# Performance work log

Measured on AMD Instinct MI355X. Metric: run time of the kernel, lower is better.

The kernel has to match this reference:

```python
import jax, jax.numpy as jnp
import numpy as np

N, F, H, E_DIM, G, NE = 20000, 128, 256, 128, 64, 320000

def _ln(x, g, b, eps=1e-5):
    m = jnp.mean(x, axis=-1, keepdims=True)
    v = jnp.mean((x - m) ** 2, axis=-1, keepdims=True)
    return (x - m) * jax.lax.rsqrt(v + eps) * g + b

def _gcn(x, src, dst, W, b, n):
    # GCNConv: h = D^{-1/2}(A+I)D^{-1/2} (x W) + b, degrees from A+I
    h = x @ W
    loop = jnp.arange(n)
    s = jnp.concatenate([src, loop])
    d = jnp.concatenate([dst, loop])
    deg = jax.ops.segment_sum(jnp.ones_like(s, dtype=h.dtype), d, num_segments=n)
    dinv = jax.lax.rsqrt(jnp.maximum(deg, 1.0))
    w_e = dinv[s] * dinv[d]  # [E+N]
    out = jax.ops.segment_sum(h[s] * w_e[:, None], d, num_segments=n)
    return out + b

def setup_inputs() -> dict:
    key = jax.random.key(0)
    ks = jax.random.split(key, 32)
    def nrm(k, shp, scale=0.05):
        return jax.random.normal(k, shp, dtype=jnp.float32) * scale
    inp = {
        'x': jax.random.normal(ks[0], (N, F), dtype=jnp.float32),
        'edge_index': jax.random.randint(ks[1], (2, NE), 0, N),
        'batch': jnp.sort(jax.random.randint(ks[2], (N,), 0, G)),
        'enc_w': nrm(ks[3], (F, H)), 'enc_b': jnp.zeros((H,), jnp.float32),
        'enc_g': jnp.ones((H,), jnp.float32), 'enc_be': jnp.zeros((H,), jnp.float32),
        'w1': nrm(ks[4], (H, H)), 'b1': jnp.zeros((H,), jnp.float32),
        'g1': jnp.ones((H,), jnp.float32), 'be1': jnp.zeros((H,), jnp.float32),
        'w2': nrm(ks[5], (H, H)), 'b2': jnp.zeros((H,), jnp.float32),
        'g2': jnp.ones((H,), jnp.float32), 'be2': jnp.zeros((H,), jnp.float32),
        'w3': nrm(ks[6], (H, H)), 'b3': jnp.zeros((H,), jnp.float32),
        'g3': jnp.ones((H,), jnp.float32), 'be3': jnp.zeros((H,), jnp.float32),
        'attn_w': nrm(ks[7], (H, 1)), 'attn_b': jnp.zeros((1,), jnp.float32),
        'pw1': nrm(ks[8], (H, H)), 'pb1': jnp.zeros((H,), jnp.float32),
        'pg': jnp.ones((H,), jnp.float32), 'pbe': jnp.zeros((H,), jnp.float32),
        'pw2': nrm(ks[9], (H, E_DIM)), 'pb2': jnp.zeros((E_DIM,), jnp.float32),
    }
    return inp

def reference(x, edge_index, batch, enc_w, enc_b, enc_g, enc_be,
              w1, b1, g1, be1, w2, b2, g2, be2, w3, b3, g3, be3,
              attn_w, attn_b, pw1, pb1, pg, pbe, pw2, pb2):
    src, dst = edge_index[0], edge_index[1]
    n = x.shape[0]
    # feature encoder (dropout = identity in eval)
    h = jax.nn.relu(_ln(x @ enc_w + enc_b, enc_g, enc_be))
    x1 = jax.nn.relu(_ln(_gcn(h, src, dst, w1, b1, n), g1, be1))
    x2 = jax.nn.relu(_ln(_gcn(x1, src, dst, w2, b2, n), g2, be2)) + x1
    x3 = jax.nn.relu(_ln(_gcn(x2, src, dst, w3, b3, n), g3, be3)) + x2
    # global softmax over the node dimension (dim=0), as in the original
    a = jnp.tanh(x3 @ attn_w + attn_b)       # [N,1]
    a = jax.nn.softmax(a, axis=0)
    pooled = jax.ops.segment_sum(x3 * a, batch, num_segments=G)  # [G,H]
    p = jax.nn.relu(_ln(pooled @ pw1 + pb1, pg, pbe))
    out = p @ pw2 + pb2                      # [G, E_DIM]
    nrm = jnp.maximum(jnp.linalg.norm(out, axis=1, keepdims=True), 1e-12)
    return out / nrm
```

## Files before the change

kernel.cpp:

```cpp
#include <hip/hip_runtime.h>
#include <hip/hip_bf16.h>

#define NN 20000
#define FF 128
#define HH 256
#define EDIM 128
#define GG 64
#define NEDGE 320000
#define PSUB 16
#define CSTRIDE 64

typedef __attribute__((ext_vector_type(4))) float f4;
typedef __attribute__((ext_vector_type(4))) float f32x4;
typedef __attribute__((ext_vector_type(8))) short bf16x8;
typedef __attribute__((ext_vector_type(4))) unsigned short u16x4;
typedef __attribute__((ext_vector_type(4))) int i32x4;

__device__ inline float wsum(float v) {
#pragma unroll
    for (int m = 32; m >= 1; m >>= 1) v += __shfl_xor(v, m, 64);
    return v;
}

__device__ inline unsigned short f2b(float f) {
    union { float f; unsigned u; } x; x.f = f;
    unsigned r = x.u + 0x7fffu + ((x.u >> 16) & 1u);
    return (unsigned short)(r >> 16);
}
__device__ inline float b2f(unsigned short u) {
    union { unsigned u; float f; } x; x.u = ((unsigned)u) << 16;
    return x.f;
}

__global__ void k_prep(const float* __restrict__ W0, const float* __restrict__ W1,
                       const float* __restrict__ W2, const float* __restrict__ W3,
                       unsigned short* __restrict__ T0, unsigned short* __restrict__ T1,
                       unsigned short* __restrict__ T2, unsigned short* __restrict__ T3,
                       int* __restrict__ cnt) {
    int b = blockIdx.x, tid = threadIdx.x;
    if (b < 20) {
        int t = b * 256 + tid;
        if (t < NN / 4) ((i32x4*)cnt)[t] = (i32x4){0, 0, 0, 0};
        return;
    }
    const float* W; unsigned short* T; int K, tt;
    if (b < 28)      { W = W0; T = T0; K = 128; tt = b - 20; }
    else if (b < 44) { W = W1; T = T1; K = 256; tt = b - 28; }
    else if (b < 60) { W = W2; T = T2; K = 256; tt = b - 44; }
    else             { W = W3; T = T3; K = 256; tt = b - 60; }
    int ktiles = K / 64;
    int kt = tt % ktiles, nt = tt / ktiles;
    int k0 = kt * 64, n0 = nt * 64;
    __shared__ unsigned short ldsT[64][65];
    int rn = (tid & 15) * 4, rk = tid >> 4;
#pragma unroll
    for (int i = 0; i < 4; i++) {
        int k = rk + 16 * i;
        f4 v = *(const f4*)(W + (size_t)(k0 + k) * 256 + n0 + rn);
#pragma unroll
        for (int j = 0; j < 4; j++) ldsT[rn + j][k] = f2b(v[j]);
    }
    __syncthreads();
    int wn = tid >> 2, kseg = (tid & 3) * 16;
#pragma unroll
    for (int q = 0; q < 4; q++) {
        u16x4 o = { ldsT[wn][kseg + q * 4 + 0], ldsT[wn][kseg + q * 4 + 1],
                    ldsT[wn][kseg + q * 4 + 2], ldsT[wn][kseg + q * 4 + 3] };
        *(u16x4*)(T + (size_t)(n0 + wn) * K + k0 + kseg + q * 4) = o;
    }
}

__global__ __launch_bounds__(256) void k_encbuild(
        const float* __restrict__ X, const unsigned short* __restrict__ Wt,
        const float* __restrict__ eb, const float* __restrict__ gam,
        const float* __restrict__ bet, unsigned short* __restrict__ outp, int M,
        const int* __restrict__ src, const int* __restrict__ dst,
        int* __restrict__ cnt, int* __restrict__ colv, int ne) {
    __shared__ unsigned short Wl[2 * 16 * 64 * 8];
    int b = blockIdx.x, tid = threadIdx.x;
    if (b >= 313) {
        int e = (b - 313) * 256 + tid;
        if (e < ne) {
            int d = dst[e];
            int pos = atomicAdd(&cnt[d], 1);
            if (pos < CSTRIDE) colv[(size_t)d * CSTRIDE + pos] = src[e];
        }
        return;
    }
    int wave = tid >> 6, lane = tid & 63;
    int lmod = lane & 15, ldiv = lane >> 4;
    int mbase = b * 64 + wave * 16;
    int row = min(mbase + lmod, M - 1);
    f32x4 acc[16] = {};
#pragma unroll
    for (int h = 0; h < 2; h++) {
        __syncthreads();
        for (int c = tid; c < 2048; c += 256) {
            int l = c & 63, nf = (c >> 6) & 15, kss = c >> 10;
            int n = nf * 16 + (l & 15);
            int k = (h * 2 + kss) * 32 + (l >> 4) * 8;
            *(bf16x8*)(Wl + (size_t)c * 8) = *(const bf16x8*)(Wt + (size_t)n * 128 + k);
        }
        __syncthreads();
#pragma unroll
        for (int kss = 0; kss < 2; kss++) {
            int ks = h * 2 + kss;
            f4 xa = *(const f4*)(X + (size_t)row * 128 + ks * 32 + ldiv * 8);
            f4 xb2 = *(const f4*)(X + (size_t)row * 128 + ks * 32 + ldiv * 8 + 4);
            bf16x8 xf;
            xf[0] = (short)f2b(xa[0]); xf[1] = (short)f2b(xa[1]);
            xf[2] = (short)f2b(xa[2]); xf[3] = (short)f2b(xa[3]);
            xf[4] = (short)f2b(xb2[0]); xf[5] = (short)f2b(xb2[1]);
            xf[6] = (short)f2b(xb2[2]); xf[7] = (short)f2b(xb2[3]);
#pragma unroll
            for (int nf = 0; nf < 16; nf++) {
                bf16x8 wf = *(bf16x8*)(Wl + ((size_t)(kss * 16 + nf) * 64 + lane) * 8);
                acc[nf] = __builtin_amdgcn_mfma_f32_16x16x32_bf16(wf, xf, acc[nf], 0, 0, 0);
            }
        }
    }
    float vs = 0.f;
#pragma unroll
    for (int nf = 0; nf < 16; nf++) {
        f4 bb = *(const f4*)(eb + nf * 16 + ldiv * 4);
#pragma unroll
        for (int r = 0; r < 4; r++) { acc[nf][r] += bb[r]; vs += acc[nf][r]; }
    }
    vs += __shfl_xor(vs, 16, 64); vs += __shfl_xor(vs, 32, 64);
    float mean = vs * (1.0f / 256.0f);
    float ss = 0.f;
#pragma unroll
    for (int nf = 0; nf < 16; nf++) {
#pragma unroll
        for (int r = 0; r < 4; r++) { float d = acc[nf][r] - mean; ss += d * d; }
    }
    ss += __shfl_xor(ss, 16, 64); ss += __shfl_xor(ss, 32, 64);
    float rs = rsqrtf(ss * (1.0f / 256.0f) + 1e-5f);
    int m = mbase + lmod;
    if (m < M) {
#pragma unroll
        for (int nf = 0; nf < 16; nf++) {
            f4 gv = *(const f4*)(gam + nf * 16 + ldiv * 4);
            f4 bv = *(const f4*)(bet + nf * 16 + ldiv * 4);
            u16x4 o;
#pragma unroll
            for (int r = 0; r < 4; r++)
                o[r] = f2b(fmaxf((acc[nf][r] - mean) * rs * gv[r] + bv[r], 0.0f));
            *(u16x4*)(outp + (size_t)m * 256 + nf * 16 + ldiv * 4) = o;
        }
    }
}

#define GEMM_NWG 628
template<int K>
__global__ __launch_bounds__(256) void bgemm(const unsigned short* __restrict__ Xb,
                                             const unsigned short* __restrict__ Wt,
                                             unsigned short* __restrict__ C, int M) {
    constexpr int KSTEPS = K / 32;
    __shared__ unsigned short Wl[KSTEPS * 4 * 64 * 8];
    int tid = threadIdx.x;
    int orig = blockIdx.y * 4 + blockIdx.x;
    int xcd = orig & 7, rest = orig >> 3;
    constexpr int q = GEMM_NWG >> 3, r = GEMM_NWG & 7;
    int wg = (xcd < r ? xcd * (q + 1) : r * (q + 1) + (xcd - r) * q) + rest;
    int m0 = wg >> 2;
    int n0 = (wg & 3) * 64;
    for (int c = tid; c < KSTEPS * 4 * 64; c += 256) {
        int lc = c & 63;
        int nf = (c >> 6) & 3;
        int ks = c >> 8;
        int n = n0 + nf * 16 + (lc & 15);
        int k = ks * 32 + (lc >> 4) * 8;
        bf16x8 v = *(const bf16x8*)(Wt + (size_t)n * K + k);
        *(bf16x8*)(Wl + (size_t)c * 8) = v;
    }
    __syncthreads();
    int wave = tid >> 6, lane = tid & 63;
    int lmod = lane & 15, ldiv = lane >> 4;
    int mbase = m0 * 128 + wave * 32;
    f32x4 acc[2][4] = {};
#pragma unroll
    for (int ks = 0; ks < KSTEPS; ks++) {
        int k0 = ks * 32 + ldiv * 8;
        bf16x8 xf[2], wf[4];
#pragma unroll
        for (int mf = 0; mf < 2; mf++) {
            int row = mbase + mf * 16 + lmod;
            row = min(row, M - 1);
            xf[mf] = *(const bf16x8*)(Xb + (size_t)row * K + k0);
        }
#pragma unroll
        for (int nf = 0; nf < 4; nf++) {
            wf[nf] = *(const bf16x8*)(Wl + ((size_t)(ks * 4 + nf) * 64 + lane) * 8);
        }
#pragma unroll
        for (int mf = 0; mf < 2; mf++) {
#pragma unroll
            for (int nf = 0; nf < 4; nf++) {
                acc[mf][nf] = __builtin_amdgcn_mfma_f32_16x16x32_bf16(
                    wf[nf], xf[mf], acc[mf][nf], 0, 0, 0);
            }
        }
    }
#pragma unroll
    for (int mf = 0; mf < 2; mf++) {
        int m = mbase + mf * 16 + lmod;
        if (m < M) {
#pragma unroll
            for (int nf = 0; nf < 4; nf++) {
                int n = n0 + nf * 16 + ldiv * 4;
                u16x4 o = { f2b(acc[mf][nf][0]), f2b(acc[mf][nf][1]),
                            f2b(acc[mf][nf][2]), f2b(acc[mf][nf][3]) };
                *(u16x4*)(C + (size_t)m * 256 + n) = o;
            }
        }
    }
}

__global__ void k_aggln(const unsigned short* __restrict__ T, const int* __restrict__ cnt,
                        const int* __restrict__ col,
                        const float* __restrict__ b, const float* __restrict__ gam,
                        const float* __restrict__ bet, const unsigned short* __restrict__ resid,
                        unsigned short* __restrict__ out,
                        const float* __restrict__ aw, const float* __restrict__ ab,
                        float* __restrict__ elog, int n) {
    int wid = (blockIdx.x * blockDim.x + threadIdx.x) >> 6;
    int lane = threadIdx.x & 63;
    if (wid >= n) return;
    int deg = min(cnt[wid], CSTRIDE);
    const int* cr = col + (size_t)wid * CSTRIDE;
    f4 a0 = {0.f,0.f,0.f,0.f}, a1 = {0.f,0.f,0.f,0.f};
    f4 a2 = {0.f,0.f,0.f,0.f}, a3 = {0.f,0.f,0.f,0.f};
    int e = 0;
    for (; e + 7 < deg; e += 8) {
        i32x4 cA = *(const i32x4*)(cr + e);
        i32x4 cB = *(const i32x4*)(cr + e + 4);
        u16x4 r0 = ((const u16x4*)(T + (size_t)cA[0] * HH))[lane];
        u16x4 r1 = ((const u16x4*)(T + (size_t)cA[1] * HH))[lane];
        u16x4 r2 = ((const u16x4*)(T + (size_t)cA[2] * HH))[lane];
        u16x4 r3 = ((const u16x4*)(T + (size_t)cA[3] * HH))[lane];
        u16x4 r4 = ((const u16x4*)(T + (size_t)cB[0] * HH))[lane];
        u16x4 r5 = ((const u16x4*)(T + (size_t)cB[1] * HH))[lane];
        u16x4 r6 = ((const u16x4*)(T + (size_t)cB[2] * HH))[lane];
        u16x4 r7 = ((const u16x4*)(T + (size_t)cB[3] * HH))[lane];
        float w0 = rsqrtf((float)(cnt[cA[0]] + 1));
        float w1 = rsqrtf((float)(cnt[cA[1]] + 1));
        float w2 = rsqrtf((float)(cnt[cA[2]] + 1));
        float w3 = rsqrtf((float)(cnt[cA[3]] + 1));
        float w4 = rsqrtf((float)(cnt[cB[0]] + 1));
        float w5 = rsqrtf((float)(cnt[cB[1]] + 1));
        float w6 = rsqrtf((float)(cnt[cB[2]] + 1));
        float w7 = rsqrtf((float)(cnt[cB[3]] + 1));
#pragma unroll
        for (int i = 0; i < 4; i++) {
            a0[i] = fmaf(w0, b2f(r0[i]), a0[i]);
            a1[i] = fmaf(w1, b2f(r1[i]), a1[i]);
            a2[i] = fmaf(w2, b2f(r2[i]), a2[i]);
            a3[i] = fmaf(w3, b2f(r3[i]), a3[i]);
            a0[i] = fmaf(w4, b2f(r4[i]), a0[i]);
            a1[i] = fmaf(w5, b2f(r5[i]), a1[i]);
            a2[i] = fmaf(w6, b2f(r6[i]), a2[i]);
            a3[i] = fmaf(w7, b2f(r7[i]), a3[i]);
        }
    }
    for (; e + 3 < deg; e += 4) {
        i32x4 c4 = *(const i32x4*)(cr + e);
        float w0 = rsqrtf((float)(cnt[c4[0]] + 1));
        float w1 = rsqrtf((float)(cnt[c4[1]] + 1));
        float w2 = rsqrtf((float)(cnt[c4[2]] + 1));
        float w3 = rsqrtf((float)(cnt[c4[3]] + 1));
        u16x4 r0 = ((const u16x4*)(T + (size_t)c4[0] * HH))[lane];
        u16x4 r1 = ((const u16x4*)(T + (size_t)c4[1] * HH))[lane];
        u16x4 r2 = ((const u16x4*)(T + (size_t)c4[2] * HH))[lane];
        u16x4 r3 = ((const u16x4*)(T + (size_t)c4[3] * HH))[lane];
#pragma unroll
        for (int i = 0; i < 4; i++) {
            a0[i] = fmaf(w0, b2f(r0[i]), a0[i]);
            a1[i] = fmaf(w1, b2f(r1[i]), a1[i]);
            a2[i] = fmaf(w2, b2f(r2[i]), a2[i]);
            a3[i] = fmaf(w3, b2f(r3[i]), a3[i]);
        }
    }
    for (; e < deg; e++) {
        int s0 = cr[e];
        float w0 = rsqrtf((float)(cnt[s0] + 1));
        u16x4 r0 = ((const u16x4*)(T + (size_t)s0 * HH))[lane];
#pragma unroll
        for (int i = 0; i < 4; i++) a0[i] = fmaf(w0, b2f(r0[i]), a0[i]);
    }
    float di = rsqrtf((float)(deg + 1));
    u16x4 sv = ((const u16x4*)(T + (size_t)wid * HH))[lane];
    f4 bb = ((const f4*)b)[lane];
    f4 v;
#pragma unroll
    for (int i = 0; i < 4; i++)
        v[i] = di * (a0[i] + a1[i] + a2[i] + a3[i]) + (di * di) * b2f(sv[i]) + bb[i];
    float s = wsum(v[0] + v[1] + v[2] + v[3]);
    float mean = s * (1.0f / HH);
    f4 d = v - mean;
    float ss = wsum(d[0] * d[0] + d[1] * d[1] + d[2] * d[2] + d[3] * d[3]);
    float rs = rsqrtf(ss * (1.0f / HH) + 1e-5f);
    f4 gv = ((const f4*)gam)[lane], bv = ((const f4*)bet)[lane];
    f4 o = d * rs * gv + bv;
#pragma unroll
    for (int i = 0; i < 4; i++) o[i] = fmaxf(o[i], 0.0f);
    if (resid != nullptr) {
        u16x4 rv = ((const u16x4*)(resid + (size_t)wid * HH))[lane];
#pragma unroll
        for (int i = 0; i < 4; i++) o[i] += b2f(rv[i]);
    }
    u16x4 ov;
#pragma unroll
    for (int i = 0; i < 4; i++) ov[i] = f2b(o[i]);
    ((u16x4*)(out + (size_t)wid * HH))[lane] = ov;
    if (elog != nullptr) {
        f4 wv = ((const f4*)aw)[lane];
        float dotv = wsum(b2f(ov[0]) * wv[0] + b2f(ov[1]) * wv[1] +
                          b2f(ov[2]) * wv[2] + b2f(ov[3]) * wv[3]);
        if (lane == 0) elog[wid] = expf(tanhf(dotv + ab[0]));
    }
}

__device__ inline int lbound(const int* __restrict__ arr, int n, int key) {
    int lo = 0, hi = n;
    while (lo < hi) {
        int mid = (lo + hi) >> 1;
        if (arr[mid] < key) lo = mid + 1; else hi = mid;
    }
    return lo;
}

__global__ __launch_bounds__(256) void k_pool(const unsigned short* __restrict__ x3,
                                              const float* __restrict__ elog,
                                              const int* __restrict__ batch,
                                              float* __restrict__ partial,
                                              float* __restrict__ esum, int n) {
    int g = blockIdx.y, s = blockIdx.x, j = threadIdx.x;
    __shared__ int slo, shi;
    if (j == 0) { slo = lbound(batch, n, g); shi = lbound(batch, n, g + 1); }
    __syncthreads();
    int lo = slo, hi = shi;
    float a0 = 0.f, a1 = 0.f;
    int i = lo + s;
    for (; i + PSUB < hi; i += 2 * PSUB) {
        a0 += elog[i] * b2f(x3[(size_t)i * HH + j]);
        a1 += elog[i + PSUB] * b2f(x3[(size_t)(i + PSUB) * HH + j]);
    }
    if (i < hi) a0 += elog[i] * b2f(x3[(size_t)i * HH + j]);
    partial[(size_t)(g * PSUB + s) * HH + j] = a0 + a1;
    if (j < 64) {
        float es = 0.f;
        for (int t = j; (size_t)lo + s + (size_t)t * PSUB < (size_t)hi; t += 64)
            es += elog[lo + s + t * PSUB];
        es = wsum(es);
        if (j == 0) esum[g * PSUB + s] = es;
    }
}

__global__ __launch_bounds__(256) void k_tail(
    const float* __restrict__ partial, const float* __restrict__ esum,
    const float* __restrict__ pw1, const float* __restrict__ pb1,
    const float* __restrict__ pg, const float* __restrict__ pbe,
    const float* __restrict__ pw2, const float* __restrict__ pb2,
    float* __restrict__ out) {
    __shared__ float pl[256];
    __shared__ float ps[256];
    __shared__ float red[256];
    __shared__ float os[128];
    int g = blockIdx.x, j = threadIdx.x;
    float t = esum[j] + esum[j + 256] + esum[j + 512] + esum[j + 768];
    red[j] = t;
    __syncthreads();
    for (int s = 128; s > 0; s >>= 1) {
        if (j < s) red[j] += red[j + s];
        __syncthreads();
    }
    float inv = 1.0f / red[0];
    __syncthreads();
    float acc = 0.f;
#pragma unroll
    for (int s = 0; s < PSUB; s++) acc += partial[(size_t)(g * PSUB + s) * HH + j];
    pl[j] = acc * inv;
    __syncthreads();
    float q = pb1[j];
#pragma unroll 8
    for (int k = 0; k < 256; k++) q = fmaf(pl[k], pw1[k * 256 + j], q);
    red[j] = q;
    __syncthreads();
    for (int s = 128; s > 0; s >>= 1) {
        if (j < s) red[j] += red[j + s];
        __syncthreads();
    }
    float mean = red[0] * (1.0f / 256.0f);
    __syncthreads();
    float d = q - mean;
    red[j] = d * d;
    __syncthreads();
    for (int s = 128; s > 0; s >>= 1) {
        if (j < s) red[j] += red[j + s];
        __syncthreads();
    }
    float var = red[0] * (1.0f / 256.0f);
    __syncthreads();
    float p = fmaxf(d * rsqrtf(var + 1e-5f) * pg[j] + pbe[j], 0.0f);
    ps[j] = p;
    __syncthreads();
    if (j < 128) {
        float o = pb2[j];
#pragma unroll 8
        for (int k = 0; k < 256; k++) o = fmaf(ps[k], pw2[k * 128 + j], o);
        os[j] = o;
    }
    __syncthreads();
    float val = (j < 128) ? os[j] * os[j] : 0.f;
    red[j] = val;
    __syncthreads();
    for (int s = 128; s > 0; s >>= 1) {
        if (j < s) red[j] += red[j + s];
        __syncthreads();
    }
    float nrm = fmaxf(sqrtf(red[0]), 1e-12f);
    if (j < 128) out[g * 128 + j] = os[j] / nrm;
}

extern "C" void kernel_launch(void* const* d_in, const int* in_sizes, int n_in,
                              void* d_out, int out_size, void* d_ws, size_t ws_size,
                              hipStream_t stream) {
    const float* x      = (const float*)d_in[0];
    const int*   ei     = (const int*)d_in[1];
    const int*   batch  = (const int*)d_in[2];
    const float* enc_w  = (const float*)d_in[3];
    const float* enc_b  = (const float*)d_in[4];
    const float* enc_g  = (const float*)d_in[5];
    const float* enc_be = (const float*)d_in[6];
    const float* w1 = (const float*)d_in[7],  *b1 = (const float*)d_in[8];
    const float* g1 = (const float*)d_in[9],  *be1 = (const float*)d_in[10];
    const float* w2 = (const float*)d_in[11], *b2 = (const float*)d_in[12];
    const float* g2 = (const float*)d_in[13], *be2 = (const float*)d_in[14];
    const float* w3 = (const float*)d_in[15], *b3 = (const float*)d_in[16];
    const float* g3 = (const float*)d_in[17], *be3 = (const float*)d_in[18];
    const float* attn_w = (const float*)d_in[19], *attn_b = (const float*)d_in[20];
    const float* pw1 = (const float*)d_in[21], *pb1 = (const float*)d_in[22];
    const float* pg  = (const float*)d_in[23], *pbe = (const float*)d_in[24];
    const float* pw2 = (const float*)d_in[25], *pb2 = (const float*)d_in[26];
    float* out = (float*)d_out;

    const int* src = ei;
    const int* dst = ei + NEDGE;

    unsigned short* us = (unsigned short*)d_ws;
    unsigned short* Tb = us;
    unsigned short* Pb = Tb + (size_t)NN * HH;
    unsigned short* Qb = Pb + (size_t)NN * HH;
    unsigned short* wte = Qb + (size_t)NN * HH;
    unsigned short* wt1 = wte + 256 * 128;
    unsigned short* wt2 = wt1 + 256 * 256;
    unsigned short* wt3 = wt2 + 256 * 256;
    float* fp = (float*)(wt3 + 256 * 256);
    float* elog    = fp;
    float* partial = elog + NN;
    float* esum    = partial + (size_t)GG * PSUB * HH;
    int* cnt = (int*)(esum + GG * PSUB);
    int* col = cnt + NN;

    k_prep<<<76, 256, 0, stream>>>(enc_w, w1, w2, w3, wte, wt1, wt2, wt3, cnt);
    k_encbuild<<<313 + 1250, 256, 0, stream>>>(x, wte, enc_b, enc_g, enc_be, Pb, NN,
                                               src, dst, cnt, col, NEDGE);

    dim3 gg(4, 157);
    bgemm<256><<<gg, 256, 0, stream>>>(Pb, wt1, Tb, NN);
    k_aggln<<<(NN + 3) / 4, 256, 0, stream>>>(Tb, cnt, col, b1, g1, be1, nullptr, Qb,
                                              nullptr, nullptr, nullptr, NN);
    bgemm<256><<<gg, 256, 0, stream>>>(Qb, wt2, Tb, NN);
    k_aggln<<<(NN + 3) / 4, 256, 0, stream>>>(Tb, cnt, col, b2, g2, be2, Qb, Pb,
                                              nullptr, nullptr, nullptr, NN);
    bgemm<256><<<gg, 256, 0, stream>>>(Pb, wt3, Tb, NN);
    k_aggln<<<(NN + 3) / 4, 256, 0, stream>>>(Tb, cnt, col, b3, g3, be3, Pb, Qb,
                                              attn_w, attn_b, elog, NN);
    k_pool<<<dim3(PSUB, GG), 256, 0, stream>>>(Qb, elog, batch, partial, esum, NN);
    k_tail<<<GG, 256, 0, stream>>>(partial, esum, pw1, pb1, pg, pbe, pw2, pb2, out);
}
```

Before: 195.9 us.

## Fuse first GCN weight GEMM into encoder kernel via swizzled LDS tile

The encoder kernel now keeps its 64-row LayerNorm+ReLU output tile in shared memory (XOR-swizzled) and multiplies it by W1 there with MFMA, writing T1 directly. This removes the separate bgemm launch and the round trip of the encoder activations through global memory. In exchange, each block uses 32KB more LDS, which can lower occupancy, and W1 fragments are read from global/L2 by every block instead of being staged once.

```diff
diff --git a/kernel.cpp b/kernel.cpp
--- a/kernel.cpp
+++ b/kernel.cpp
@@ -70,13 +70,15 @@
     }
 }
 
-__global__ __launch_bounds__(256) void k_encbuild(
+__global__ __launch_bounds__(256) void k_encg1(
         const float* __restrict__ X, const unsigned short* __restrict__ Wt,
+        const unsigned short* __restrict__ Wt1,
         const float* __restrict__ eb, const float* __restrict__ gam,
-        const float* __restrict__ bet, unsigned short* __restrict__ outp, int M,
+        const float* __restrict__ bet, unsigned short* __restrict__ T1out, int M,
         const int* __restrict__ src, const int* __restrict__ dst,
         int* __restrict__ cnt, int* __restrict__ colv, int ne) {
     __shared__ unsigned short Wl[2 * 16 * 64 * 8];
+    __shared__ unsigned short hs[64 * 256];
     int b = blockIdx.x, tid = threadIdx.x;
     if (b >= 313) {
         int e = (b - 313) * 256 + tid;
@@ -136,17 +138,54 @@
     }
     ss += __shfl_xor(ss, 16, 64); ss += __shfl_xor(ss, 32, 64);
     float rs = rsqrtf(ss * (1.0f / 256.0f) + 1e-5f);
-    int m = mbase + lmod;
-    if (m < M) {
-#pragma unroll
-        for (int nf = 0; nf < 16; nf++) {
-            f4 gv = *(const f4*)(gam + nf * 16 + ldiv * 4);
-            f4 bv = *(const f4*)(bet + nf * 16 + ldiv * 4);
-            u16x4 o;
-#pragma unroll
-            for (int r = 0; r < 4; r++)
-                o[r] = f2b(fmaxf((acc[nf][r] - mean) * rs * gv[r] + bv[r], 0.0f));
-            *(u16x4*)(outp + (size_t)m * 256 + nf * 16 + ldiv * 4) = o;
+    int r_loc = wave * 16 + lmod;
+    int swz = (r_loc & 7) << 4;
+#pragma unroll
+    for (int nf = 0; nf < 16; nf++) {
+        f4 gv = *(const f4*)(gam + nf * 16 + ldiv * 4);
+        f4 bv = *(const f4*)(bet + nf * 16 + ldiv * 4);
+        u16x4 o;
+#pragma unroll
+        for (int r = 0; r < 4; r++)
+            o[r] = f2b(fmaxf((acc[nf][r] - mean) * rs * gv[r] + bv[r], 0.0f));
+        int byte = ((nf * 32 + ldiv * 8) ^ swz);
+        *(u16x4*)((char*)hs + (size_t)r_loc * 512 + byte) = o;
+    }
+    __syncthreads();
+    f32x4 acc2[4][4] = {};
+    const unsigned short* wb = Wt1 + (size_t)(wave * 64 + lmod) * 256 + ldiv * 8;
+#pragma unroll
+    for (int ks = 0; ks < 8; ks++) {
+        bf16x8 wf[4], hf[4];
+#pragma unroll
+        for (int nf = 0; nf < 4; nf++)
+            wf[nf] = *(const bf16x8*)(wb + (size_t)nf * 16 * 256 + ks * 32);
+#pragma unroll
+        for (int rg = 0; rg < 4; rg++) {
+            int rr = rg * 16 + lmod;
+            int byte = ((ks * 64 + ldiv * 16) ^ ((rr & 7) << 4));
+            hf[rg] = *(const bf16x8*)((const char*)hs + (size_t)rr * 512 + byte);
+        }
+#pragma unroll
+        for (int rg = 0; rg < 4; rg++) {
+#pragma unroll
+            for (int nf = 0; nf < 4; nf++) {
+                acc2[rg][nf] = __builtin_amdgcn_mfma_f32_16x16x32_bf16(
+                    wf[nf], hf[rg], acc2[rg][nf], 0, 0, 0);
+            }
+        }
+    }
+#pragma unroll
+    for (int rg = 0; rg < 4; rg++) {
+        int m = b * 64 + rg * 16 + lmod;
+        if (m < M) {
+#pragma unroll
+            for (int nf = 0; nf < 4; nf++) {
+                int n = wave * 64 + nf * 16 + ldiv * 4;
+                u16x4 o = { f2b(acc2[rg][nf][0]), f2b(acc2[rg][nf][1]),
+                            f2b(acc2[rg][nf][2]), f2b(acc2[rg][nf][3]) };
+                *(u16x4*)(T1out + (size_t)m * 256 + n) = o;
+            }
         }
     }
 }
@@ -464,11 +503,10 @@
     int* col = cnt + NN;
 
     k_prep<<<76, 256, 0, stream>>>(enc_w, w1, w2, w3, wte, wt1, wt2, wt3, cnt);
-    k_encbuild<<<313 + 1250, 256, 0, stream>>>(x, wte, enc_b, enc_g, enc_be, Pb, NN,
-                                               src, dst, cnt, col, NEDGE);
+    k_encg1<<<313 + 1250, 256, 0, stream>>>(x, wte, wt1, enc_b, enc_g, enc_be, Tb, NN,
+                                            src, dst, cnt, col, NEDGE);
 
     dim3 gg(4, 157);
-    bgemm<256><<<gg, 256, 0, stream>>>(Pb, wt1, Tb, NN);
     k_aggln<<<(NN + 3) / 4, 256, 0, stream>>>(Tb, cnt, col, b1, g1, be1, nullptr, Qb,
                                               nullptr, nullptr, nullptr, NN);
     bgemm<256><<<gg, 256, 0, stream>>>(Qb, wt2, Tb, NN);
```

Measured after the change: 183.1 us (median of 2 runs). 1.07x faster.
